# Optimization experiments

Measured on AMD Instinct MI355X. Metric: run time of the kernel, lower is better.

Reference implementation:

```python
import jax, jax.numpy as jnp
import numpy as np

B_, L_, D_MODEL, D_STATE, EXPAND, D_CONV = 4, 2048, 1024, 16, 2, 4
D_INNER = EXPAND * D_MODEL          # 2048
DT_RANK = (D_MODEL + 15) // 16      # 64


def setup_inputs() -> dict:
    key = jax.random.key(0)
    ks = jax.random.split(key, 8)
    s = lambda k, shape, scale: jax.random.normal(k, shape, jnp.float32) * scale
    return {
        "u": jax.random.normal(ks[0], (B_, L_, D_MODEL), jnp.float32),
        "hiddens": jnp.zeros((B_, D_INNER, D_STATE), jnp.float32),  # initial SSM state h0
        "in_proj_w": s(ks[1], (D_MODEL, 2 * D_INNER), D_MODEL ** -0.5),
        "conv_w": s(ks[2], (D_INNER, 1, D_CONV), D_CONV ** -0.5),   # depthwise kernel (O,I/g,K)
        "conv_b": jnp.zeros((D_INNER,), jnp.float32),
        "x_proj_w": s(ks[3], (D_INNER, DT_RANK + 2 * D_STATE), D_INNER ** -0.5),
        "dt_proj_w": s(ks[4], (DT_RANK, D_INNER), DT_RANK ** -0.5),
        "dt_proj_b": jnp.log(jnp.expm1(jnp.full((D_INNER,), 0.01, jnp.float32))),  # softplus^-1(0.01)
        "A_log": jnp.log(jnp.tile(jnp.arange(1, D_STATE + 1, dtype=jnp.float32), (D_INNER, 1))),
        "D": jnp.ones((D_INNER,), jnp.float32),
        "out_proj_w": s(ks[5], (D_INNER, D_MODEL), D_INNER ** -0.5),
        "training": 0,
    }


def reference(u, hiddens, in_proj_w, conv_w, conv_b, x_proj_w, dt_proj_w,
              dt_proj_b, A_log, D, out_proj_w, training):
    # --- input projection -> (x, res) ---
    x, res = jnp.split(u @ in_proj_w, 2, axis=-1)           # each [b, l, d_inner]

    # --- depthwise causal conv1d (width D_CONV) + silu ---
    xc = jax.lax.conv_general_dilated(
        x.transpose(0, 2, 1), conv_w, (1,), [(D_CONV - 1, 0)],
        dimension_numbers=('NCH', 'OIH', 'NCH'), feature_group_count=D_INNER)
    x = jax.nn.silu((xc + conv_b[None, :, None]).transpose(0, 2, 1))  # [b, l, d_inner]

    # --- data-dependent SSM parameters ---
    dbc = x @ x_proj_w                                       # [b, l, dt_rank + 2n]
    delta = jax.nn.softplus(dbc[..., :DT_RANK] @ dt_proj_w + dt_proj_b)  # [b, l, d_inner]
    Bm = dbc[..., DT_RANK:DT_RANK + D_STATE]                 # [b, l, n]
    Cm = dbc[..., DT_RANK + D_STATE:]                        # [b, l, n]
    A = -jnp.exp(A_log)                                      # [d_inner, n]

    # --- selective scan over time ---
    def step(h, inp):
        dt, Bt, Ct, ut = inp                                 # [b,d], [b,n], [b,n], [b,d]
        dA = jnp.exp(dt[:, :, None] * A)                     # [b, d, n]
        h = dA * h + dt[:, :, None] * Bt[:, None, :] * ut[:, :, None]
        y = jnp.einsum('bdn,bn->bd', h, Ct)
        return h, y

    xs = (delta.transpose(1, 0, 2), Bm.transpose(1, 0, 2),
          Cm.transpose(1, 0, 2), x.transpose(1, 0, 2))
    _, ys = jax.lax.scan(step, hiddens, xs)                  # ys: [l, b, d_inner]

    y = ys.transpose(1, 0, 2) + x * D                        # skip via D
    y = y * jax.nn.silu(res)                                 # gated output
    return y @ out_proj_w                                    # [b, l, d_model]
```

## Files before the change

kernel.cpp:

```cpp
#include <hip/hip_runtime.h>
#include <hip/hip_bf16.h>
#include <cstddef>

#define B_   4
#define L_   2048
#define DM   1024
#define DI   2048
#define NST  16
#define DTR  64
#define NBC  96
#define NTOK 8192

using bf16 = __hip_bfloat16;
typedef __attribute__((ext_vector_type(8))) short bf16x8;
typedef __attribute__((ext_vector_type(4))) short s16x4;
typedef __attribute__((ext_vector_type(4))) float f32x4;

__device__ __forceinline__ float bf2f(short s) {
  unsigned u = ((unsigned)(unsigned short)s) << 16;
  float f; __builtin_memcpy(&f, &u, 4); return f;
}
__device__ __forceinline__ short f2bs(float f) {
  __hip_bfloat16 h = __float2bfloat16(f);
  short s; __builtin_memcpy(&s, &h, 2); return s;
}
__device__ __forceinline__ float sigmoidf_fast(float x) {
  return 1.f / (1.f + __expf(-x));
}

#define GLD16(g, l) __builtin_amdgcn_global_load_lds( \
  (const __attribute__((address_space(1))) unsigned int*)(g), \
  (__attribute__((address_space(3))) unsigned int*)(l), 16, 0, 0)

__device__ __forceinline__ float swz_xor8(float x) {
  return __builtin_bit_cast(float,
    __builtin_amdgcn_ds_swizzle(__builtin_bit_cast(int, x), 0x201F));
}
__device__ __forceinline__ float swz_xor4(float x) {
  return __builtin_bit_cast(float,
    __builtin_amdgcn_ds_swizzle(__builtin_bit_cast(int, x), 0x101F));
}
template<int CTRL>
__device__ __forceinline__ float qperm(float x) {
  return __builtin_bit_cast(float,
    __builtin_amdgcn_update_dpp(0, __builtin_bit_cast(int, x), CTRL, 0xf, 0xf, false));
}
template<int S>
__device__ __forceinline__ float swz_bcast16(float x) {
  return __builtin_bit_cast(float,
    __builtin_amdgcn_ds_swizzle(__builtin_bit_cast(int, x), (S << 5) | 0x10));
}

__device__ __forceinline__ void transpose_tile(
    const float* __restrict__ in, short* __restrict__ out,
    int R, int Cc, int lin, int lout, int bx, int by, int tid, short (*t)[33])
{
  const int r0 = bx * 32, c0 = by * 32;
  const int tx = tid & 31, ty = tid >> 5;
#pragma unroll
  for (int i = 0; i < 4; i++) {
    int r = r0 + ty + i * 8;
    int c = c0 + tx;
    short v = 0;
    if (r < R && c < Cc) v = f2bs(in[(size_t)r * lin + c]);
    t[ty + i * 8][tx] = v;
  }
  __syncthreads();
#pragma unroll
  for (int i = 0; i < 4; i++) {
    int c = c0 + ty + i * 8;
    int r = r0 + tx;
    if (c < Cc && r < lout) out[(size_t)c * lout + r] = t[tx][ty + i * 8];
  }
}

__global__ __launch_bounds__(256)
void prep(const float* __restrict__ u, short* __restrict__ ub,
          const float* __restrict__ in_proj, short* __restrict__ Wt1,
          const float* __restrict__ x_proj, short* __restrict__ Wxp,
          const float* __restrict__ dt_proj, short* __restrict__ dtw)
{
  __shared__ short t[32][33];
  int id = blockIdx.x;
  const int tid = threadIdx.x;
  if (id < 4096) {
    const size_t i = ((size_t)id * 256 + tid) * 8;
    float4 a0 = *(const float4*)(u + i);
    float4 a1 = *(const float4*)(u + i + 4);
    union { bf16x8 v; short h[8]; } o;
    o.h[0] = f2bs(a0.x); o.h[1] = f2bs(a0.y); o.h[2] = f2bs(a0.z); o.h[3] = f2bs(a0.w);
    o.h[4] = f2bs(a1.x); o.h[5] = f2bs(a1.y); o.h[6] = f2bs(a1.z); o.h[7] = f2bs(a1.w);
    *(bf16x8*)(ub + i) = o.v;
    return;
  }
  id -= 4096;
  if (id < 4096) {
    transpose_tile(in_proj, Wt1, 1024, 4096, 4096, 1024, id & 31, id >> 5, tid, t);
    return;
  }
  id -= 4096;
  if (id < 192) {
    transpose_tile(x_proj, Wxp, 2048, 96, 96, 2048, id % 64, id / 64, tid, t);
    return;
  }
  id -= 192;
  transpose_tile(dt_proj, dtw, 64, 2048, 2048, 64, id & 1, id >> 1, tid, t);
}

__global__ __launch_bounds__(256)
void gemm_bt(const short* __restrict__ A, const short* __restrict__ Bt,
             void* __restrict__ Cv, void* __restrict__ Cv2, const float* __restrict__ bias,
             int N, int K, int lda, int ldb, int ldc, int ldc2, int mode)
{
  __shared__ short As[128][64];
  __shared__ short Bs[128][64];
  const int gx = gridDim.x, gy = gridDim.y;
  const int nwg = gx * gy;
  const int lid = blockIdx.x + gx * blockIdx.y;
  const int cpx = nwg >> 3;
  const int swz = (lid & 7) * cpx + (lid >> 3);
  const int nig = gy << 3;
  const int grp_ = swz / nig;
  const int ing = swz - grp_ * nig;
  const int m0 = (grp_ * 8 + (ing & 7)) * 128;
  const int n0 = (ing >> 3) * 128;
  const int tid  = threadIdx.x;
  const int wave = tid >> 6, lane = tid & 63;
  const int wr = (wave >> 1) * 64, wc = (wave & 1) * 64;
  const int la = lane & 15, gq = lane >> 4;
  const int rs = (la & 7) << 3;
  f32x4 acc[4][4] = {};

  for (int k0 = 0; k0 < K; k0 += 64) {
#pragma unroll
    for (int i = 0; i < 4; i++) {
      int idx = tid + i * 256;
      int row = idx >> 3, kc = (idx & 7) * 8;
      int kcs = kc ^ ((row & 7) << 3);
      GLD16(A  + (size_t)(m0 + row) * lda + k0 + kcs, &As[row][kc]);
      GLD16(Bt + (size_t)(n0 + row) * ldb + k0 + kcs, &Bs[row][kc]);
    }
    __syncthreads();
#pragma unroll
    for (int kk = 0; kk < 2; kk++) {
      const int cl = (kk * 32 + gq * 8) ^ rs;
      bf16x8 af[4], bfr[4];
#pragma unroll
      for (int i = 0; i < 4; i++) af[i]  = *(const bf16x8*)(&As[wr + i * 16 + la][cl]);
#pragma unroll
      for (int j = 0; j < 4; j++) bfr[j] = *(const bf16x8*)(&Bs[wc + j * 16 + la][cl]);
#pragma unroll
      for (int i = 0; i < 4; i++)
#pragma unroll
        for (int j = 0; j < 4; j++)
          acc[i][j] = __builtin_amdgcn_mfma_f32_16x16x32_bf16(af[i], bfr[j], acc[i][j], 0, 0, 0);
    }
    __syncthreads();
  }

#pragma unroll
  for (int i = 0; i < 4; i++) {
    int rowb = m0 + wr + i * 16 + gq * 4;
#pragma unroll
    for (int j = 0; j < 4; j++) {
      int col = n0 + wc + j * 16 + la;
      if (col >= N) continue;
      if (mode == 2) {
#pragma unroll
        for (int r = 0; r < 4; r++)
          ((float*)Cv)[(size_t)(rowb + r) * ldc + col] = acc[i][j][r];
      } else if (mode == 4) {
        if (col < DTR) {
#pragma unroll
          for (int r = 0; r < 4; r++)
            ((short*)Cv)[(size_t)(rowb + r) * ldc + col] = f2bs(acc[i][j][r]);
        } else {
          s16x4 pk;
#pragma unroll
          for (int r = 0; r < 4; r++) pk[r] = f2bs(acc[i][j][r]);
          *(s16x4*)((short*)Cv2 + (size_t)(col - DTR) * ldc2 + rowb) = pk;
        }
      } else if (mode == 5) {
        short* base = (col < DI) ? (short*)Cv : (short*)Cv2;
        int c = (col < DI) ? col : col - DI;
        int ld = (col < DI) ? ldc : ldc2;
#pragma unroll
        for (int r = 0; r < 4; r++)
          base[(size_t)(rowb + r) * ld + c] = f2bs(acc[i][j][r]);
      } else if (mode == 6) {
#pragma unroll
        for (int r = 0; r < 4; r++) {
          float v = acc[i][j][r] + bias[rowb + r];
          float e = exp2f(v * 1.44269504f);
          v = (v > 20.f) ? v : 0.69314718f * __log2f(1.f + e);
          ((short*)Cv)[(size_t)(rowb + r) * ldc + col] = f2bs(v);
        }
      } else {
#pragma unroll
        for (int r = 0; r < 4; r++)
          ((short*)Cv)[(size_t)(rowb + r) * ldc + col] = f2bs(acc[i][j][r]);
      }
    }
  }
}

__global__ __launch_bounds__(256)
void conv_silu(const short* __restrict__ xb, const float* __restrict__ cw,
               const float* __restrict__ cb, short* __restrict__ xs,
               const float* __restrict__ op, short* __restrict__ Wt4)
{
  __shared__ short t[32][33];
  const int blk = blockIdx.x;
  if (blk >= NTOK) {
    const int id2 = blk - NTOK;
    transpose_tile(op, Wt4, 2048, 1024, 1024, 2048, id2 & 63, id2 >> 6, threadIdx.x, t);
    return;
  }
  const int token = blk;
  const int l = token & (L_ - 1);
  const int d0 = threadIdx.x * 8;

  float w[32];
#pragma unroll
  for (int i = 0; i < 8; i++) {
    float4 tw = *(const float4*)(cw + (size_t)(d0 + i) * 4);
    w[i * 4 + 0] = tw.x; w[i * 4 + 1] = tw.y; w[i * 4 + 2] = tw.z; w[i * 4 + 3] = tw.w;
  }
  float acc[8];
  {
    float4 b0 = *(const float4*)(cb + d0);
    float4 b1 = *(const float4*)(cb + d0 + 4);
    acc[0] = b0.x; acc[1] = b0.y; acc[2] = b0.z; acc[3] = b0.w;
    acc[4] = b1.x; acc[5] = b1.y; acc[6] = b1.z; acc[7] = b1.w;
  }
#pragma unroll
  for (int j = 0; j < 4; j++) {
    int lj = l - 3 + j;
    if (lj >= 0) {
      bf16x8 xv = *(const bf16x8*)(xb + (size_t)(token - 3 + j) * DI + d0);
#pragma unroll
      for (int i = 0; i < 8; i++) acc[i] += w[i * 4 + j] * bf2f(xv[i]);
    }
  }
  union { bf16x8 v; short h[8]; } o;
#pragma unroll
  for (int i = 0; i < 8; i++) {
    float v = acc[i];
    o.h[i] = f2bs(v * sigmoidf_fast(v));
  }
  *(bf16x8*)(xs + (size_t)token * DI + d0) = o.v;
}

__global__ __launch_bounds__(512, 1)
void scan_kernel(const short* __restrict__ dT, const short* __restrict__ dbcT,
                 const short* __restrict__ xs, short* __restrict__ resy,
                 const float* __restrict__ A_log, const float* __restrict__ Dw,
                 const float* __restrict__ h0)
{
  const int lane = threadIdx.x & 63;
  const int grp = threadIdx.x >> 4, n = threadIdx.x & 15;
  const int ch = blockIdx.x * 32 + grp;
  const int b = ch >> 11, d = ch & (DI - 1);
  const bool b3 = (lane & 8) != 0, b2 = (lane & 4) != 0,
             b1 = (lane & 2) != 0, b0 = (lane & 1) != 0;
  const float An2 = -__expf(A_log[d * NST + n]) * 1.44269504f;
  const float Dd = Dw[d];
  float h = h0[(size_t)ch * NST + n];

  const size_t t0 = (size_t)b * L_;
  const short* dRow = dT   + (size_t)d * NTOK + t0;
  const short* bRow = dbcT + (size_t)n * NTOK + t0;
  const short* cRow = bRow + (size_t)NST * NTOK;
  const short* uLn  = xs   + (t0 + n) * DI + d;
  short*       yCol = resy + (t0 + n) * DI + d;

  auto LOADB = [&](int lv, bf16x8& t0v, bf16x8& t1v, bf16x8& B0v, bf16x8& B1v,
                   bf16x8& C0v, bf16x8& C1v, short& uo, short& rr) {
    t0v = *(const bf16x8*)(dRow + lv);
    t1v = *(const bf16x8*)(dRow + lv + 8);
    B0v = *(const bf16x8*)(bRow + lv);
    B1v = *(const bf16x8*)(bRow + lv + 8);
    C0v = *(const bf16x8*)(cRow + lv);
    C1v = *(const bf16x8*)(cRow + lv + 8);
    uo = uLn[(size_t)lv * DI];
    rr = yCol[(size_t)lv * DI];
  };

  auto STEP = [&](int lv, bf16x8 t0v, bf16x8 t1v, bf16x8 B0v, bf16x8 B1v,
                  bf16x8 C0v, bf16x8 C1v, short uo, short rr) {
    const float uown = bf2f(uo);
    __builtin_amdgcn_s_setprio(1);
    float uf[16];
    uf[0]  = swz_bcast16<0>(uown);   uf[1]  = swz_bcast16<1>(uown);
    uf[2]  = swz_bcast16<2>(uown);   uf[3]  = swz_bcast16<3>(uown);
    uf[4]  = swz_bcast16<4>(uown);   uf[5]  = swz_bcast16<5>(uown);
    uf[6]  = swz_bcast16<6>(uown);   uf[7]  = swz_bcast16<7>(uown);
    uf[8]  = swz_bcast16<8>(uown);   uf[9]  = swz_bcast16<9>(uown);
    uf[10] = swz_bcast16<10>(uown);  uf[11] = swz_bcast16<11>(uown);
    uf[12] = swz_bcast16<12>(uown);  uf[13] = swz_bcast16<13>(uown);
    uf[14] = swz_bcast16<14>(uown);  uf[15] = swz_bcast16<15>(uown);
    float dA[16], w[16];
#pragma unroll
    for (int s = 0; s < 16; s++) {
      float dt = bf2f(s < 8 ? t0v[s] : t1v[s - 8]);
      dA[s] = exp2f(dt * An2);
      w[s]  = dt * uf[s] * bf2f(s < 8 ? B0v[s] : B1v[s - 8]);
    }
    float p[16];
#pragma unroll
    for (int s = 0; s < 16; s++) {
      h = __builtin_fmaf(dA[s], h, w[s]);
      p[s] = h * bf2f(s < 8 ? C0v[s] : C1v[s - 8]);
    }
    float q8[8];
#pragma unroll
    for (int i = 0; i < 8; i++) {
      float keep = b3 ? p[i + 8] : p[i];
      float send = b3 ? p[i]     : p[i + 8];
      q8[i] = keep + swz_xor8(send);
    }
    float q4[4];
#pragma unroll
    for (int i = 0; i < 4; i++) {
      float keep = b2 ? q8[i + 4] : q8[i];
      float send = b2 ? q8[i]     : q8[i + 4];
      q4[i] = keep + swz_xor4(send);
    }
    float q2[2];
#pragma unroll
    for (int i = 0; i < 2; i++) {
      float keep = b1 ? q4[i + 2] : q4[i];
      float send = b1 ? q4[i]     : q4[i + 2];
      q2[i] = keep + qperm<0x4E>(send);
    }
    float keep = b0 ? q2[1] : q2[0];
    float send = b0 ? q2[0] : q2[1];
    float ysum = keep + qperm<0xB1>(send);
    ysum = __builtin_fmaf(uown, Dd, ysum);
    float r = bf2f(rr);
    float yv = ysum * (r * sigmoidf_fast(r));
    __builtin_amdgcn_s_setprio(0);
    yCol[(size_t)lv * DI] = f2bs(yv);
  };

  bf16x8 a0, a1, a2, a3, a4, a5; short ua, ra;
  bf16x8 c0, c1, c2, c3, c4, c5; short ub, rb;
  LOADB(0, a0, a1, a2, a3, a4, a5, ua, ra);
  for (int l = 0; l < L_; l += 32) {
    LOADB(l + 16, c0, c1, c2, c3, c4, c5, ub, rb);
    STEP(l, a0, a1, a2, a3, a4, a5, ua, ra);
    if (l + 32 < L_) LOADB(l + 32, a0, a1, a2, a3, a4, a5, ua, ra);
    STEP(l + 16, c0, c1, c2, c3, c4, c5, ub, rb);
  }
}

extern "C" void kernel_launch(void* const* d_in, const int* in_sizes, int n_in,
                              void* d_out, int out_size, void* d_ws, size_t ws_size,
                              hipStream_t stream)
{
  const float* u        = (const float*)d_in[0];
  const float* hiddens  = (const float*)d_in[1];
  const float* in_proj  = (const float*)d_in[2];
  const float* conv_w   = (const float*)d_in[3];
  const float* conv_b   = (const float*)d_in[4];
  const float* x_proj   = (const float*)d_in[5];
  const float* dt_proj  = (const float*)d_in[6];
  const float* dt_bias  = (const float*)d_in[7];
  const float* A_log    = (const float*)d_in[8];
  const float* Dw       = (const float*)d_in[9];
  const float* out_proj = (const float*)d_in[10];
  float* out = (float*)d_out;

  char* w = (char*)d_ws;
  short* Wt1  = (short*)w;
  short* Wt4  = Wt1;
  w += (size_t)4096 * 1024 * 2;
  short* Wxp  = (short*)w; w += (size_t)128  * 2048 * 2;
  short* dtw  = (short*)w; w += (size_t)2048 * 64   * 2;
  short* xbuf = (short*)w; w += (size_t)NTOK * DI   * 2;
  short* resy = (short*)w; w += (size_t)NTOK * DI   * 2;
  short* dbc  = (short*)w; w += (size_t)NTOK * DTR  * 2;
  short* dbcT = (short*)w; w += (size_t)32   * NTOK * 2;
  short* ub   = (short*)d_out;
  short* xs   = (short*)d_out;
  short* dT   = xbuf;

  prep<<<4096 + 4096 + 192 + 128, 256, 0, stream>>>(u, ub, in_proj, Wt1,
                                                    x_proj, Wxp, dt_proj, dtw);

  gemm_bt<<<dim3(64, 32), 256, 0, stream>>>(ub, Wt1, xbuf, resy, nullptr,
                                            4096, 1024, 1024, 1024, DI, DI, 5);
  conv_silu<<<NTOK + 2048, 256, 0, stream>>>(xbuf, conv_w, conv_b, xs, out_proj, Wt4);
  gemm_bt<<<dim3(64, 1), 256, 0, stream>>>(xs, Wxp, dbc, dbcT, nullptr,
                                           96, 2048, 2048, 2048, DTR, NTOK, 4);
  gemm_bt<<<dim3(16, 64), 256, 0, stream>>>(dtw, dbc, dT, nullptr, dt_bias,
                                            NTOK, 64, 64, 64, NTOK, 0, 6);
  scan_kernel<<<256, 512, 0, stream>>>(dT, dbcT, xs, resy, A_log, Dw, hiddens);
  gemm_bt<<<dim3(64, 8), 256, 0, stream>>>(resy, Wt4, out, nullptr, nullptr,
                                           1024, 2048, 2048, 2048, 1024, 0, 2);
}
```

Before: 592.3 us.

## Add 256x256 double-buffered swizzled GEMM for in_proj and out_proj

Introduces a 512-thread GEMM kernel with 256x256 tiles, double-buffered XOR-swizzled LDS, and next-tile global loads interleaved with MFMA issue using priority hints. It replaces the 128x128 single-buffered GEMM for the input and output projections, aiming for more operand reuse and overlap of memory and compute. The large tile uses 128 KB of LDS, so only one block fits per CU. The output projection launches only 128 blocks, which can leave CUs idle.

After: 614.2 us. 3.7% more time.

```diff
diff --git a/kernel.cpp b/kernel.cpp
--- a/kernel.cpp
+++ b/kernel.cpp
@@ -105,6 +105,105 @@
   }
   id -= 192;
   transpose_tile(dt_proj, dtw, 64, 2048, 2048, 64, id & 1, id >> 1, tid, t);
+}
+
+__global__ __launch_bounds__(512, 2)
+void gemm256(const short* __restrict__ A, const short* __restrict__ Bt,
+             void* __restrict__ Cv, void* __restrict__ Cv2,
+             int N, int K, int lda, int ldb, int ldc, int ldc2, int mode)
+{
+  __shared__ short As[2][256][64];
+  __shared__ short Bs[2][256][64];
+  const int gx = gridDim.x, gy = gridDim.y;
+  const int nwg = gx * gy;
+  const int lid = blockIdx.x + gx * blockIdx.y;
+  const int cpx = nwg >> 3;
+  const int swz = (lid & 7) * cpx + (lid >> 3);
+  const int nig = gy << 2;
+  const int grp_ = swz / nig;
+  const int ing = swz - grp_ * nig;
+  const int m0 = (grp_ * 4 + (ing & 3)) * 256;
+  const int n0 = (ing >> 2) * 256;
+
+  const int tid  = threadIdx.x;
+  const int wid  = tid >> 6, lane = tid & 63;
+  const int wm = wid >> 2, wn = wid & 3;
+  const int la = lane & 15, gq = lane >> 4;
+  const int rowA0 = wm * 128 + la;
+  const int rowB0 = wn * 64 + la;
+  const int rs = (la & 7) << 3;
+  f32x4 acc[8][4] = {};
+
+  auto STAGE1 = [&](int buf, int k0, int Lq) {
+    int idx = tid + Lq * 512;
+    int row = idx >> 3, kc8 = (idx & 7) * 8;
+    int kcs = kc8 ^ ((row & 7) << 3);
+    GLD16(A  + (size_t)(m0 + row) * lda + k0 + kcs, &As[buf][row][kc8]);
+    GLD16(Bt + (size_t)(n0 + row) * ldb + k0 + kcs, &Bs[buf][row][kc8]);
+  };
+
+#pragma unroll
+  for (int q = 0; q < 4; q++) STAGE1(0, 0, q);
+  asm volatile("s_waitcnt vmcnt(0) lgkmcnt(0)" ::: "memory");
+  __builtin_amdgcn_s_barrier();
+  __builtin_amdgcn_sched_barrier(0);
+
+  const int NT = K >> 6;
+  int cur = 0;
+  for (int kt = 0; kt < NT; kt++) {
+    const int knext = (kt + 1) << 6;
+    const bool pf = (kt + 1 < NT);
+    bf16x8 bfr[4][2];
+#pragma unroll
+    for (int j = 0; j < 4; j++)
+#pragma unroll
+      for (int ks = 0; ks < 2; ks++)
+        bfr[j][ks] = *(const bf16x8*)(&Bs[cur][rowB0 + j * 16][(ks * 32 + gq * 8) ^ rs]);
+#pragma unroll
+    for (int q = 0; q < 4; q++) {
+      if (pf) STAGE1(cur ^ 1, knext, q);
+      bf16x8 af[2][2];
+#pragma unroll
+      for (int r = 0; r < 2; r++)
+#pragma unroll
+        for (int ks = 0; ks < 2; ks++)
+          af[r][ks] = *(const bf16x8*)(&As[cur][rowA0 + (2 * q + r) * 16][(ks * 32 + gq * 8) ^ rs]);
+      __builtin_amdgcn_s_setprio(1);
+#pragma unroll
+      for (int r = 0; r < 2; r++)
+#pragma unroll
+        for (int j = 0; j < 4; j++) {
+          acc[2 * q + r][j] = __builtin_amdgcn_mfma_f32_16x16x32_bf16(af[r][0], bfr[j][0], acc[2 * q + r][j], 0, 0, 0);
+          acc[2 * q + r][j] = __builtin_amdgcn_mfma_f32_16x16x32_bf16(af[r][1], bfr[j][1], acc[2 * q + r][j], 0, 0, 0);
+        }
+      __builtin_amdgcn_s_setprio(0);
+    }
+    asm volatile("s_waitcnt vmcnt(0) lgkmcnt(0)" ::: "memory");
+    __builtin_amdgcn_s_barrier();
+    __builtin_amdgcn_sched_barrier(0);
+    cur ^= 1;
+  }
+
+#pragma unroll
+  for (int i = 0; i < 8; i++) {
+    int rowb = m0 + wm * 128 + i * 16 + gq * 4;
+#pragma unroll
+    for (int j = 0; j < 4; j++) {
+      int col = n0 + wn * 64 + j * 16 + la;
+      if (mode == 2) {
+#pragma unroll
+        for (int r = 0; r < 4; r++)
+          ((float*)Cv)[(size_t)(rowb + r) * ldc + col] = acc[i][j][r];
+      } else {
+        short* base = (col < DI) ? (short*)Cv : (short*)Cv2;
+        int c = (col < DI) ? col : col - DI;
+        int ld = (col < DI) ? ldc : ldc2;
+#pragma unroll
+        for (int r = 0; r < 4; r++)
+          base[(size_t)(rowb + r) * ld + c] = f2bs(acc[i][j][r]);
+      }
+    }
+  }
 }
 
 __global__ __launch_bounds__(256)
@@ -165,11 +264,7 @@
     for (int j = 0; j < 4; j++) {
       int col = n0 + wc + j * 16 + la;
       if (col >= N) continue;
-      if (mode == 2) {
-#pragma unroll
-        for (int r = 0; r < 4; r++)
-          ((float*)Cv)[(size_t)(rowb + r) * ldc + col] = acc[i][j][r];
-      } else if (mode == 4) {
+      if (mode == 4) {
         if (col < DTR) {
 #pragma unroll
           for (int r = 0; r < 4; r++)
@@ -180,13 +275,6 @@
           for (int r = 0; r < 4; r++) pk[r] = f2bs(acc[i][j][r]);
           *(s16x4*)((short*)Cv2 + (size_t)(col - DTR) * ldc2 + rowb) = pk;
         }
-      } else if (mode == 5) {
-        short* base = (col < DI) ? (short*)Cv : (short*)Cv2;
-        int c = (col < DI) ? col : col - DI;
-        int ld = (col < DI) ? ldc : ldc2;
-#pragma unroll
-        for (int r = 0; r < 4; r++)
-          base[(size_t)(rowb + r) * ld + c] = f2bs(acc[i][j][r]);
       } else if (mode == 6) {
 #pragma unroll
         for (int r = 0; r < 4; r++) {
@@ -388,7 +476,7 @@
   prep<<<4096 + 4096 + 192 + 128, 256, 0, stream>>>(u, ub, in_proj, Wt1,
                                                     x_proj, Wxp, dt_proj, dtw);
 
-  gemm_bt<<<dim3(64, 32), 256, 0, stream>>>(ub, Wt1, xbuf, resy, nullptr,
+  gemm256<<<dim3(32, 16), 512, 0, stream>>>(ub, Wt1, xbuf, resy,
                                             4096, 1024, 1024, 1024, DI, DI, 5);
   conv_silu<<<NTOK + 2048, 256, 0, stream>>>(xbuf, conv_w, conv_b, xs, out_proj, Wt4);
   gemm_bt<<<dim3(64, 1), 256, 0, stream>>>(xs, Wxp, dbc, dbcT, nullptr,
@@ -396,6 +484,6 @@
   gemm_bt<<<dim3(16, 64), 256, 0, stream>>>(dtw, dbc, dT, nullptr, dt_bias,
                                             NTOK, 64, 64, 64, NTOK, 0, 6);
   scan_kernel<<<256, 512, 0, stream>>>(dT, dbcT, xs, resy, A_log, Dw, hiddens);
-  gemm_bt<<<dim3(64, 8), 256, 0, stream>>>(resy, Wt4, out, nullptr, nullptr,
+  gemm256<<<dim3(32, 4), 512, 0, stream>>>(resy, Wt4, out, nullptr,
                                            1024, 2048, 2048, 2048, 1024, 0, 2);
 }
```
